# Kernel optimization log

Hardware: AMD Instinct MI355X
Metric: run time of the kernel (lower is better)

Reference implementation:

```python
import jax, jax.numpy as jnp
import numpy as np

STEP = 5
ALPHA = 0.01
D = 1024
BN_EPS = 1e-5
L2_EPS = 1e-12


def setup_inputs() -> dict:
    key = jax.random.key(0)
    k1, k2 = jax.random.split(key, 2)
    B = 16
    x = jax.random.normal(k1, (B * STEP, D), dtype=jnp.float32)
    W = jax.random.normal(k2, (D, D), dtype=jnp.float32) * 0.02
    b = jnp.zeros((D,), jnp.float32)
    gamma = jnp.ones((D,), jnp.float32)
    beta = jnp.zeros((D,), jnp.float32)
    return {"x": x, "W": W, "b": b, "gamma": gamma, "beta": beta}


def reference(x, W, b, gamma, beta):
    BS = x.shape[0]          # B * STEP
    B = BS // STEP
    x_seq = x.reshape(B, STEP, D)

    def step_fn(h, xt):
        # xt: [B, D]; Hebbian fast-weight update
        # hebb = alpha * (k v^T - k^2 * h)
        hebb = ALPHA * (xt[:, :, None] * xt[:, None, :] - (xt ** 2)[:, :, None] * h)
        h = h + hebb
        return h, h

    h0 = jnp.zeros((B, D, D), x.dtype)
    _, mems = jax.lax.scan(step_fn, h0, jnp.swapaxes(x_seq, 0, 1))  # [STEP, B, D, D]
    # torch.cat(memory_total, dim=0) -> step-major stacking
    mem = mems.reshape(BS, D, D)

    # batched mat-vec readout; x here is batch-major (faithful to original mismatch)
    q = jnp.einsum('nij,nj->ni', mem, x)  # [BS, D]

    y = q @ W.T + b
    # BatchNorm1d in training mode: batch statistics, biased variance
    mu = y.mean(axis=0)
    var = y.var(axis=0)
    yhat = (y - mu) / jnp.sqrt(var + BN_EPS)
    out = jax.nn.relu(yhat * gamma + beta)
    # F.normalize: L2 over dim=1 with eps clamp
    norm = jnp.linalg.norm(out, axis=1, keepdims=True)
    return out / jnp.maximum(norm, L2_EPS)
```

## Files before the change

### kernel.cpp

```cpp
#include <hip/hip_runtime.h>
#include <math.h>

#define D_DIM   1024
#define BS      80
#define STEPS   5
#define ALPHA   0.01f
#define BN_EPS  1e-5f
#define L2_EPS  1e-12f

#define NG      8
#define NROWS   10
#define JBLK    128
#define G_BLOCKS (NG * JBLK)

__global__ __launch_bounds__(256) void kQ(const float* __restrict__ x,
                                          float* __restrict__ q) {
    const int n    = blockIdx.x;
    const int tid  = threadIdx.x;
    const int lane = tid & 63;
    const int wid  = tid >> 6;
    const int t    = n >> 4;
    const int bb   = n & 15;

    const float4* __restrict__ xv = (const float4*)(x + (size_t)n * D_DIM);
    const float4 v = xv[tid];

    float4 k[STEPS];
#pragma unroll
    for (int s = 0; s < STEPS; ++s)
        k[s] = ((const float4*)(x + (size_t)(bb * STEPS + s) * D_DIM))[tid];

    float p[STEPS];
#pragma unroll
    for (int s = 0; s < STEPS; ++s)
        p[s] = k[s].x * v.x + k[s].y * v.y + k[s].z * v.z + k[s].w * v.w;

#pragma unroll
    for (int off = 32; off; off >>= 1) {
#pragma unroll
        for (int s = 0; s < STEPS; ++s) p[s] += __shfl_xor(p[s], off, 64);
    }

    __shared__ float sh[4][STEPS];
    if (lane == 0) {
#pragma unroll
        for (int s = 0; s < STEPS; ++s) sh[wid][s] = p[s];
    }
    __syncthreads();
    float c[STEPS];
#pragma unroll
    for (int s = 0; s < STEPS; ++s)
        c[s] = sh[0][s] + sh[1][s] + sh[2][s] + sh[3][s];

    float4 acc = make_float4(0.f, 0.f, 0.f, 0.f);
    for (int s = 0; s <= t; ++s) {
        const float4 xs = k[s];
        acc.x = acc.x * (1.f - ALPHA * xs.x * xs.x) + c[s] * xs.x;
        acc.y = acc.y * (1.f - ALPHA * xs.y * xs.y) + c[s] * xs.y;
        acc.z = acc.z * (1.f - ALPHA * xs.z * xs.z) + c[s] * xs.z;
        acc.w = acc.w * (1.f - ALPHA * xs.w * xs.w) + c[s] * xs.w;
    }
    acc.x *= ALPHA; acc.y *= ALPHA; acc.z *= ALPHA; acc.w *= ALPHA;
    ((float4*)(q + (size_t)n * D_DIM))[tid] = acc;
}

__global__ __launch_bounds__(256, 4) void kG(const float* __restrict__ q,
                                             const float* __restrict__ W,
                                             const float* __restrict__ bvec,
                                             float* __restrict__ y,
                                             float* __restrict__ psum,
                                             float* __restrict__ psq) {
    const int tid  = threadIdx.x;
    const int lane = tid & 63;
    const int wid  = tid >> 6;
    const int bid  = blockIdx.x;
    const int ng   = bid >> 7;
    const int jb   = bid & 127;
    const int j0   = jb * 8;
    const int n0   = ng * NROWS;
    const int jw   = j0 + wid * 2;

    __shared__ float qs[NROWS][D_DIM];

    const float4* __restrict__ W4 = (const float4*)W;
    float4 w[2][4];
#pragma unroll
    for (int jj = 0; jj < 2; ++jj)
#pragma unroll
        for (int m = 0; m < 4; ++m)
            w[jj][m] = W4[(size_t)(jw + jj) * 256 + lane + 64 * m];
    const float b0 = bvec[jw];
    const float b1 = bvec[jw + 1];

    {
        const float4* __restrict__ q4 = (const float4*)(q + (size_t)n0 * D_DIM);
        float4* __restrict__ qs4 = (float4*)qs;
#pragma unroll
        for (int i = 0; i < (NROWS * 256) / 256; ++i)
            qs4[tid + 256 * i] = q4[tid + 256 * i];
    }
    __syncthreads();

    float csum[2] = {0.f, 0.f};
    float csq [2] = {0.f, 0.f};

#pragma unroll 2
    for (int nn = 0; nn < NROWS; ++nn) {
        const int n = n0 + nn;
        float4 qv[4];
#pragma unroll
        for (int m = 0; m < 4; ++m)
            qv[m] = ((const float4*)qs[nn])[lane + 64 * m];

        float s0 = 0.f, s1 = 0.f;
#pragma unroll
        for (int m = 0; m < 4; ++m) {
            s0 += w[0][m].x * qv[m].x + w[0][m].y * qv[m].y
                + w[0][m].z * qv[m].z + w[0][m].w * qv[m].w;
            s1 += w[1][m].x * qv[m].x + w[1][m].y * qv[m].y
                + w[1][m].z * qv[m].z + w[1][m].w * qv[m].w;
        }
#pragma unroll
        for (int off = 32; off; off >>= 1) {
            s0 += __shfl_xor(s0, off, 64);
            s1 += __shfl_xor(s1, off, 64);
        }
        if (lane == 0) {
            const float y0 = s0 + b0;
            const float y1 = s1 + b1;
            ((float2*)(y + (size_t)n * D_DIM + jw))[0] = make_float2(y0, y1);
            csum[0] += y0; csum[1] += y1;
            csq [0] += y0 * y0; csq [1] += y1 * y1;
        }
    }
    if (lane == 0) {
        ((float2*)(psum + (size_t)ng * D_DIM + jw))[0] = make_float2(csum[0], csum[1]);
        ((float2*)(psq  + (size_t)ng * D_DIM + jw))[0] = make_float2(csq [0], csq [1]);
    }
}

__global__ __launch_bounds__(256) void kB(const float* __restrict__ y,
                                          const float* __restrict__ psum,
                                          const float* __restrict__ psq,
                                          const float* __restrict__ gamma,
                                          const float* __restrict__ beta,
                                          float* __restrict__ out) {
    const int n   = blockIdx.x;
    const int tid = threadIdx.x;

    float4 su = make_float4(0.f, 0.f, 0.f, 0.f);
    float4 sq = make_float4(0.f, 0.f, 0.f, 0.f);
#pragma unroll
    for (int g = 0; g < NG; ++g) {
        const float4 a = ((const float4*)psum)[g * 256 + tid];
        const float4 b = ((const float4*)psq )[g * 256 + tid];
        su.x += a.x; su.y += a.y; su.z += a.z; su.w += a.w;
        sq.x += b.x; sq.y += b.y; sq.z += b.z; sq.w += b.w;
    }
    const float inv_bs = 1.f / (float)BS;
    const float4 yv = ((const float4*)y)[(size_t)n * 256 + tid];
    const float4 g4 = ((const float4*)gamma)[tid];
    const float4 be = ((const float4*)beta)[tid];

    float4 o;
    {
        const float mu = su.x * inv_bs;
        const float istd = rsqrtf(sq.x * inv_bs - mu * mu + BN_EPS);
        o.x = fmaxf((yv.x - mu) * istd * g4.x + be.x, 0.f);
    }
    {
        const float mu = su.y * inv_bs;
        const float istd = rsqrtf(sq.y * inv_bs - mu * mu + BN_EPS);
        o.y = fmaxf((yv.y - mu) * istd * g4.y + be.y, 0.f);
    }
    {
        const float mu = su.z * inv_bs;
        const float istd = rsqrtf(sq.z * inv_bs - mu * mu + BN_EPS);
        o.z = fmaxf((yv.z - mu) * istd * g4.z + be.z, 0.f);
    }
    {
        const float mu = su.w * inv_bs;
        const float istd = rsqrtf(sq.w * inv_bs - mu * mu + BN_EPS);
        o.w = fmaxf((yv.w - mu) * istd * g4.w + be.w, 0.f);
    }

    float ss = o.x * o.x + o.y * o.y + o.z * o.z + o.w * o.w;
#pragma unroll
    for (int off = 32; off; off >>= 1) ss += __shfl_xor(ss, off, 64);
    __shared__ float sred[4];
    if ((tid & 63) == 0) sred[tid >> 6] = ss;
    __syncthreads();
    const float stot = sred[0] + sred[1] + sred[2] + sred[3];

    const float scale = 1.f / fmaxf(sqrtf(stot), L2_EPS);
    float4 ov = make_float4(o.x * scale, o.y * scale, o.z * scale, o.w * scale);
    ((float4*)out)[(size_t)n * 256 + tid] = ov;
}

extern "C" void kernel_launch(void* const* d_in, const int* in_sizes, int n_in,
                              void* d_out, int out_size, void* d_ws, size_t ws_size,
                              hipStream_t stream) {
    const float* x     = (const float*)d_in[0];
    const float* W     = (const float*)d_in[1];
    const float* bvec  = (const float*)d_in[2];
    const float* gamma = (const float*)d_in[3];
    const float* beta  = (const float*)d_in[4];

    float* q    = (float*)d_ws;
    float* y    = q + BS * D_DIM;
    float* psum = y + BS * D_DIM;
    float* psq  = psum + NG * D_DIM;

    float* out = (float*)d_out;

    kQ<<<BS,       256, 0, stream>>>(x, q);
    kG<<<G_BLOCKS, 256, 0, stream>>>(q, W, bvec, y, psum, psq);
    kB<<<BS,       256, 0, stream>>>(y, psum, psq, gamma, beta, out);
}
```

Measured before the change: 78.91 us.

## Fuse BatchNorm/L2 normalize into GEMV kernel via atomic grid barrier

Removes the separate kB launch. The first 80 blocks of kG wait on 64 strided atomic counters, reset in kQ, until all GEMV blocks have published their partial sums, then perform the BN+ReLU+L2 normalization. This saves one kernel launch and its gap. It relies on the waiting blocks not starving the other blocks of the 1024-block grid, and the spinning adds some polling cost.

```diff
diff --git a/kernel.cpp b/kernel.cpp
--- a/kernel.cpp
+++ b/kernel.cpp
@@ -13,14 +13,21 @@
 #define JBLK    128
 #define G_BLOCKS (NG * JBLK)
 
+#define NCTR       64
+#define CTR_STRIDE 32
+#define BLK_PER_CTR (G_BLOCKS / NCTR)
+
 __global__ __launch_bounds__(256) void kQ(const float* __restrict__ x,
-                                          float* __restrict__ q) {
+                                          float* __restrict__ q,
+                                          int* __restrict__ ctr) {
     const int n    = blockIdx.x;
     const int tid  = threadIdx.x;
     const int lane = tid & 63;
     const int wid  = tid >> 6;
     const int t    = n >> 4;
     const int bb   = n & 15;
+
+    if (n == 0 && tid < NCTR) ctr[tid * CTR_STRIDE] = 0;
 
     const float4* __restrict__ xv = (const float4*)(x + (size_t)n * D_DIM);
     const float4 v = xv[tid];
@@ -69,7 +76,11 @@
                                              const float* __restrict__ bvec,
                                              float* __restrict__ y,
                                              float* __restrict__ psum,
-                                             float* __restrict__ psq) {
+                                             float* __restrict__ psq,
+                                             int* __restrict__ ctr,
+                                             const float* __restrict__ gamma,
+                                             const float* __restrict__ beta,
+                                             float* __restrict__ out) {
     const int tid  = threadIdx.x;
     const int lane = tid & 63;
     const int wid  = tid >> 6;
@@ -137,64 +148,75 @@
         ((float2*)(psum + (size_t)ng * D_DIM + jw))[0] = make_float2(csum[0], csum[1]);
         ((float2*)(psq  + (size_t)ng * D_DIM + jw))[0] = make_float2(csq [0], csq [1]);
     }
-}
-
-__global__ __launch_bounds__(256) void kB(const float* __restrict__ y,
-                                          const float* __restrict__ psum,
-                                          const float* __restrict__ psq,
-                                          const float* __restrict__ gamma,
-                                          const float* __restrict__ beta,
-                                          float* __restrict__ out) {
-    const int n   = blockIdx.x;
-    const int tid = threadIdx.x;
-
-    float4 su = make_float4(0.f, 0.f, 0.f, 0.f);
-    float4 sq = make_float4(0.f, 0.f, 0.f, 0.f);
-#pragma unroll
-    for (int g = 0; g < NG; ++g) {
-        const float4 a = ((const float4*)psum)[g * 256 + tid];
-        const float4 b = ((const float4*)psq )[g * 256 + tid];
-        su.x += a.x; su.y += a.y; su.z += a.z; su.w += a.w;
-        sq.x += b.x; sq.y += b.y; sq.z += b.z; sq.w += b.w;
-    }
-    const float inv_bs = 1.f / (float)BS;
-    const float4 yv = ((const float4*)y)[(size_t)n * 256 + tid];
-    const float4 g4 = ((const float4*)gamma)[tid];
-    const float4 be = ((const float4*)beta)[tid];
-
-    float4 o;
+
+    __threadfence();
+    __syncthreads();
+    if (tid == 0)
+        __hip_atomic_fetch_add(&ctr[(bid >> 4) * CTR_STRIDE], 1,
+                               __ATOMIC_RELEASE, __HIP_MEMORY_SCOPE_AGENT);
+
+    if (bid >= BS) return;
+
+    if (wid == 0) {
+        while (__hip_atomic_load(&ctr[lane * CTR_STRIDE],
+                                 __ATOMIC_ACQUIRE, __HIP_MEMORY_SCOPE_AGENT)
+               < BLK_PER_CTR)
+            __builtin_amdgcn_s_sleep(16);
+    }
+    __syncthreads();
+    __threadfence();
+
     {
-        const float mu = su.x * inv_bs;
-        const float istd = rsqrtf(sq.x * inv_bs - mu * mu + BN_EPS);
-        o.x = fmaxf((yv.x - mu) * istd * g4.x + be.x, 0.f);
-    }
-    {
-        const float mu = su.y * inv_bs;
-        const float istd = rsqrtf(sq.y * inv_bs - mu * mu + BN_EPS);
-        o.y = fmaxf((yv.y - mu) * istd * g4.y + be.y, 0.f);
-    }
-    {
-        const float mu = su.z * inv_bs;
-        const float istd = rsqrtf(sq.z * inv_bs - mu * mu + BN_EPS);
-        o.z = fmaxf((yv.z - mu) * istd * g4.z + be.z, 0.f);
-    }
-    {
-        const float mu = su.w * inv_bs;
-        const float istd = rsqrtf(sq.w * inv_bs - mu * mu + BN_EPS);
-        o.w = fmaxf((yv.w - mu) * istd * g4.w + be.w, 0.f);
-    }
-
-    float ss = o.x * o.x + o.y * o.y + o.z * o.z + o.w * o.w;
-#pragma unroll
-    for (int off = 32; off; off >>= 1) ss += __shfl_xor(ss, off, 64);
-    __shared__ float sred[4];
-    if ((tid & 63) == 0) sred[tid >> 6] = ss;
-    __syncthreads();
-    const float stot = sred[0] + sred[1] + sred[2] + sred[3];
-
-    const float scale = 1.f / fmaxf(sqrtf(stot), L2_EPS);
-    float4 ov = make_float4(o.x * scale, o.y * scale, o.z * scale, o.w * scale);
-    ((float4*)out)[(size_t)n * 256 + tid] = ov;
+        const int n = bid;
+
+        float4 su = make_float4(0.f, 0.f, 0.f, 0.f);
+        float4 sq = make_float4(0.f, 0.f, 0.f, 0.f);
+#pragma unroll
+        for (int g = 0; g < NG; ++g) {
+            const float4 a = ((const float4*)psum)[g * 256 + tid];
+            const float4 b = ((const float4*)psq )[g * 256 + tid];
+            su.x += a.x; su.y += a.y; su.z += a.z; su.w += a.w;
+            sq.x += b.x; sq.y += b.y; sq.z += b.z; sq.w += b.w;
+        }
+        const float inv_bs = 1.f / (float)BS;
+        const float4 yv = ((const float4*)y)[(size_t)n * 256 + tid];
+        const float4 g4 = ((const float4*)gamma)[tid];
+        const float4 be = ((const float4*)beta)[tid];
+
+        float4 o;
+        {
+            const float mu = su.x * inv_bs;
+            const float istd = rsqrtf(sq.x * inv_bs - mu * mu + BN_EPS);
+            o.x = fmaxf((yv.x - mu) * istd * g4.x + be.x, 0.f);
+        }
+        {
+            const float mu = su.y * inv_bs;
+            const float istd = rsqrtf(sq.y * inv_bs - mu * mu + BN_EPS);
+            o.y = fmaxf((yv.y - mu) * istd * g4.y + be.y, 0.f);
+        }
+        {
+            const float mu = su.z * inv_bs;
+            const float istd = rsqrtf(sq.z * inv_bs - mu * mu + BN_EPS);
+            o.z = fmaxf((yv.z - mu) * istd * g4.z + be.z, 0.f);
+        }
+        {
+            const float mu = su.w * inv_bs;
+            const float istd = rsqrtf(sq.w * inv_bs - mu * mu + BN_EPS);
+            o.w = fmaxf((yv.w - mu) * istd * g4.w + be.w, 0.f);
+        }
+
+        float ss = o.x * o.x + o.y * o.y + o.z * o.z + o.w * o.w;
+#pragma unroll
+        for (int off = 32; off; off >>= 1) ss += __shfl_xor(ss, off, 64);
+        __shared__ float sred[4];
+        if (lane == 0) sred[wid] = ss;
+        __syncthreads();
+        const float stot = sred[0] + sred[1] + sred[2] + sred[3];
+
+        const float scale = 1.f / fmaxf(sqrtf(stot), L2_EPS);
+        float4 ov = make_float4(o.x * scale, o.y * scale, o.z * scale, o.w * scale);
+        ((float4*)out)[(size_t)n * 256 + tid] = ov;
+    }
 }
 
 extern "C" void kernel_launch(void* const* d_in, const int* in_sizes, int n_in,
@@ -210,10 +232,11 @@
     float* y    = q + BS * D_DIM;
     float* psum = y + BS * D_DIM;
     float* psq  = psum + NG * D_DIM;
+    int*   ctr  = (int*)(psq + NG * D_DIM);
 
     float* out = (float*)d_out;
 
-    kQ<<<BS,       256, 0, stream>>>(x, q);
-    kG<<<G_BLOCKS, 256, 0, stream>>>(q, W, bvec, y, psum, psq);
-    kB<<<BS,       256, 0, stream>>>(y, psum, psq, gamma, beta, out);
+    kQ<<<BS,       256, 0, stream>>>(x, q, ctr);
+    kG<<<G_BLOCKS, 256, 0, stream>>>(q, W, bvec, y, psum, psq, ctr,
+                                     gamma, beta, out);
 }
```

Result: slower. 173.6 us (+120.0%).

## Retile GEMV kernel to 4 output columns per wave and 5 rows per block

Applied to the files above, without the earlier changes.

The y = qW^T+b kernel now has each wave hold 4 W rows in registers instead of 2, and each block covers 16 output columns over 5 q rows instead of 8 columns over 10 rows. The block count stays at 1024, but there are 16 row groups of partial BN statistics instead of 8. The aim is more FMAs per shared-memory q load, fewer shuffles per output, and vector float4 stores. In exchange W is re-read from global/L2 twice as often (16 row groups vs 8), register pressure goes up, and the BN kernel sums twice as many partial rows.

```diff
diff --git a/kernel.cpp b/kernel.cpp
--- a/kernel.cpp
+++ b/kernel.cpp
@@ -8,10 +8,10 @@
 #define BN_EPS  1e-5f
 #define L2_EPS  1e-12f
 
-#define NG      8
-#define NROWS   10
-#define JBLK    128
-#define G_BLOCKS (NG * JBLK)
+#define NGH     16
+#define NROWS   5
+#define JBLK    64
+#define G_BLOCKS (NGH * JBLK)
 
 __global__ __launch_bounds__(256) void kQ(const float* __restrict__ x,
                                           float* __restrict__ q) {
@@ -74,37 +74,34 @@
     const int lane = tid & 63;
     const int wid  = tid >> 6;
     const int bid  = blockIdx.x;
-    const int ng   = bid >> 7;
-    const int jb   = bid & 127;
-    const int j0   = jb * 8;
-    const int n0   = ng * NROWS;
-    const int jw   = j0 + wid * 2;
+    const int ngh  = bid >> 6;
+    const int jb   = bid & 63;
+    const int n0   = ngh * NROWS;
+    const int jw   = jb * 16 + wid * 4;
 
     __shared__ float qs[NROWS][D_DIM];
 
     const float4* __restrict__ W4 = (const float4*)W;
-    float4 w[2][4];
-#pragma unroll
-    for (int jj = 0; jj < 2; ++jj)
+    float4 w[4][4];
+#pragma unroll
+    for (int jj = 0; jj < 4; ++jj)
 #pragma unroll
         for (int m = 0; m < 4; ++m)
             w[jj][m] = W4[(size_t)(jw + jj) * 256 + lane + 64 * m];
-    const float b0 = bvec[jw];
-    const float b1 = bvec[jw + 1];
+    const float4 b4 = *(const float4*)(bvec + jw);
 
     {
         const float4* __restrict__ q4 = (const float4*)(q + (size_t)n0 * D_DIM);
         float4* __restrict__ qs4 = (float4*)qs;
 #pragma unroll
-        for (int i = 0; i < (NROWS * 256) / 256; ++i)
+        for (int i = 0; i < NROWS; ++i)
             qs4[tid + 256 * i] = q4[tid + 256 * i];
     }
     __syncthreads();
 
-    float csum[2] = {0.f, 0.f};
-    float csq [2] = {0.f, 0.f};
-
-#pragma unroll 2
+    float csum[4] = {0.f, 0.f, 0.f, 0.f};
+    float csq [4] = {0.f, 0.f, 0.f, 0.f};
+
     for (int nn = 0; nn < NROWS; ++nn) {
         const int n = n0 + nn;
         float4 qv[4];
@@ -112,30 +109,34 @@
         for (int m = 0; m < 4; ++m)
             qv[m] = ((const float4*)qs[nn])[lane + 64 * m];
 
-        float s0 = 0.f, s1 = 0.f;
-#pragma unroll
-        for (int m = 0; m < 4; ++m) {
-            s0 += w[0][m].x * qv[m].x + w[0][m].y * qv[m].y
-                + w[0][m].z * qv[m].z + w[0][m].w * qv[m].w;
-            s1 += w[1][m].x * qv[m].x + w[1][m].y * qv[m].y
-                + w[1][m].z * qv[m].z + w[1][m].w * qv[m].w;
+        float s[4] = {0.f, 0.f, 0.f, 0.f};
+#pragma unroll
+        for (int jj = 0; jj < 4; ++jj) {
+#pragma unroll
+            for (int m = 0; m < 4; ++m) {
+                s[jj] += w[jj][m].x * qv[m].x + w[jj][m].y * qv[m].y
+                       + w[jj][m].z * qv[m].z + w[jj][m].w * qv[m].w;
+            }
         }
 #pragma unroll
         for (int off = 32; off; off >>= 1) {
-            s0 += __shfl_xor(s0, off, 64);
-            s1 += __shfl_xor(s1, off, 64);
+#pragma unroll
+            for (int jj = 0; jj < 4; ++jj) s[jj] += __shfl_xor(s[jj], off, 64);
         }
         if (lane == 0) {
-            const float y0 = s0 + b0;
-            const float y1 = s1 + b1;
-            ((float2*)(y + (size_t)n * D_DIM + jw))[0] = make_float2(y0, y1);
-            csum[0] += y0; csum[1] += y1;
-            csq [0] += y0 * y0; csq [1] += y1 * y1;
+            float4 yv = make_float4(s[0] + b4.x, s[1] + b4.y,
+                                    s[2] + b4.z, s[3] + b4.w);
+            *(float4*)(y + (size_t)n * D_DIM + jw) = yv;
+            csum[0] += yv.x; csum[1] += yv.y; csum[2] += yv.z; csum[3] += yv.w;
+            csq[0] += yv.x * yv.x; csq[1] += yv.y * yv.y;
+            csq[2] += yv.z * yv.z; csq[3] += yv.w * yv.w;
         }
     }
     if (lane == 0) {
-        ((float2*)(psum + (size_t)ng * D_DIM + jw))[0] = make_float2(csum[0], csum[1]);
-        ((float2*)(psq  + (size_t)ng * D_DIM + jw))[0] = make_float2(csq [0], csq [1]);
+        *(float4*)(psum + (size_t)ngh * D_DIM + jw) =
+            make_float4(csum[0], csum[1], csum[2], csum[3]);
+        *(float4*)(psq  + (size_t)ngh * D_DIM + jw) =
+            make_float4(csq[0], csq[1], csq[2], csq[3]);
     }
 }
 
@@ -151,7 +152,7 @@
     float4 su = make_float4(0.f, 0.f, 0.f, 0.f);
     float4 sq = make_float4(0.f, 0.f, 0.f, 0.f);
 #pragma unroll
-    for (int g = 0; g < NG; ++g) {
+    for (int g = 0; g < NGH; ++g) {
         const float4 a = ((const float4*)psum)[g * 256 + tid];
         const float4 b = ((const float4*)psq )[g * 256 + tid];
         su.x += a.x; su.y += a.y; su.z += a.z; su.w += a.w;
@@ -209,7 +210,7 @@
     float* q    = (float*)d_ws;
     float* y    = q + BS * D_DIM;
     float* psum = y + BS * D_DIM;
-    float* psq  = psum + NG * D_DIM;
+    float* psq  = psum + NGH * D_DIM;
 
     float* out = (float*)d_out;
 
```

Result: no change. 78.65 us (-0.3%).
